# Kernel optimization log

Hardware: AMD Instinct MI355X
Metric: run time of the kernel (lower is better)

## Reference

```python
import math
import jax, jax.numpy as jnp
import numpy as np

D_MODEL = 512
N_HEADS = 8
NUM_PHASES = 3
LN_EPS = 1e-5


def setup_inputs() -> dict:
    key = jax.random.key(0)
    ks = jax.random.split(key, 8)
    B, T, C = 4, 2048, D_MODEL
    s = 1.0 / math.sqrt(C)  # keep activations sane
    return {
        "x": jax.random.normal(ks[0], (B, T, C), dtype=jnp.float32),
        "Wq_w": jax.random.normal(ks[1], (C, C), dtype=jnp.float32) * s,
        "Wq_b": jnp.zeros((C,), dtype=jnp.float32),
        "Wk_w": jax.random.normal(ks[2], (C, C), dtype=jnp.float32) * s,
        "Wk_b": jnp.zeros((C,), dtype=jnp.float32),
        "Wv_w": jax.random.normal(ks[3], (C, C), dtype=jnp.float32) * s,
        "Wv_b": jnp.zeros((C,), dtype=jnp.float32),
        "Wo_w": jax.random.normal(ks[4], (C, C), dtype=jnp.float32) * s,
        "Wo_b": jnp.zeros((C,), dtype=jnp.float32),
        "phase_bias": jax.random.normal(ks[5], (NUM_PHASES, NUM_PHASES), dtype=jnp.float32),
        "ln_g": jnp.ones((C,), dtype=jnp.float32),
        "ln_b": jnp.zeros((C,), dtype=jnp.float32),
    }


def reference(x, Wq_w, Wq_b, Wk_w, Wk_b, Wv_w, Wv_b, Wo_w, Wo_b, phase_bias, ln_g, ln_b):
    B, T, C = x.shape
    H, dk = N_HEADS, C // N_HEADS
    # torch Linear: y = x @ W.T + b
    Q = (x @ Wq_w.T + Wq_b).reshape(B, T, H, dk).transpose(0, 2, 1, 3)
    K = (x @ Wk_w.T + Wk_b).reshape(B, T, H, dk).transpose(0, 2, 1, 3)
    V = (x @ Wv_w.T + Wv_b).reshape(B, T, H, dk).transpose(0, 2, 1, 3)
    scores = jnp.einsum('bhqd,bhkd->bhqk', Q, K) / math.sqrt(dk)  # [B,H,T,T]
    # tiled additive phase bias (num_phases <= T)
    n_tiles = (T + NUM_PHASES - 1) // NUM_PHASES
    bias = jnp.tile(phase_bias, (n_tiles, n_tiles))[:T, :T]  # [T,T]
    scores = scores + bias  # broadcast over B,H
    attn = jax.nn.softmax(scores, axis=-1)  # dropout is identity in eval
    ctx = jnp.einsum('bhqk,bhkd->bhqd', attn, V)
    ctx = ctx.transpose(0, 2, 1, 3).reshape(B, T, C)
    out = ctx @ Wo_w.T + Wo_b
    y = out + x
    mu = jnp.mean(y, axis=-1, keepdims=True)
    var = jnp.mean(jnp.square(y - mu), axis=-1, keepdims=True)
    return (y - mu) / jnp.sqrt(var + LN_EPS) * ln_g + ln_b
```

## Files before the change

### kernel.cpp

```cpp
#include <hip/hip_runtime.h>

typedef __attribute__((ext_vector_type(8))) short s16x8;
typedef __attribute__((ext_vector_type(8))) unsigned short u16x8;
typedef __attribute__((ext_vector_type(4))) float f32x4;
typedef unsigned short u16;
typedef unsigned int u32;

#define T_ 2048
#define C_ 512
#define H_ 8
#define DKP 128
#define LOG2E 1.44269504088896340736f
#define QSCALE 0.18033688011112042f

__device__ __forceinline__ u16 f2b(float f) {
  u32 u = __float_as_uint(f);
  return (u16)((u + 0x7FFFu + ((u >> 16) & 1u)) >> 16);
}

__device__ __forceinline__ float b2f(u16 b) {
  return __uint_as_float(((u32)b) << 16);
}

__device__ __forceinline__ u32 cvtpk(float a, float b) {
  u32 d;
  asm("v_cvt_pk_bf16_f32 %0, %1, %2" : "=v"(d) : "v"(a), "v"(b));
  return d;
}

__device__ __forceinline__ u16x8 cvt8(float4 a, float4 b) {
  u16x8 o;
  o[0] = f2b(a.x); o[1] = f2b(a.y); o[2] = f2b(a.z); o[3] = f2b(a.w);
  o[4] = f2b(b.x); o[5] = f2b(b.y); o[6] = f2b(b.z); o[7] = f2b(b.w);
  return o;
}

__device__ __forceinline__ f32x4 mfma16(s16x8 a, s16x8 b, f32x4 c) {
  return __builtin_amdgcn_mfma_f32_16x16x32_bf16(a, b, c, 0, 0, 0);
}

#define GLL(gp, lp) __builtin_amdgcn_global_load_lds( \
    (const __attribute__((address_space(1))) unsigned int*)(gp), \
    (__attribute__((address_space(3))) unsigned int*)(lp), 16, 0, 0)

__global__ __launch_bounds__(256) void k_convert(
    const float* __restrict__ x,
    const float* __restrict__ wq, const float* __restrict__ wk,
    const float* __restrict__ wv, const float* __restrict__ wo,
    const float* __restrict__ bq, const float* __restrict__ bk,
    const float* __restrict__ bv, const float* __restrict__ pb,
    u16* __restrict__ xb, u16* __restrict__ wcat, u16* __restrict__ wo16,
    float* __restrict__ bcat, u16* __restrict__ qp, u16* __restrict__ kp)
{
  const int blk = blockIdx.x, tid = threadIdx.x;
  if (blk < 2048) {
    int i = blk * 2048 + tid * 8;
    float4 a = *(const float4*)(x + i);
    float4 b = *(const float4*)(x + i + 4);
    *(u16x8*)(xb + i) = cvt8(a, b);
  } else if (blk < 2432) {
    int bi = blk - 2048;
    const float* src; int off;
    if (bi < 128)      { src = wq; off = bi * 2048; }
    else if (bi < 256) { src = wk; off = (bi - 128) * 2048; }
    else               { src = wv; off = (bi - 256) * 2048; }
    int i = off + tid * 8;
    float4 a = *(const float4*)(src + i);
    float4 b = *(const float4*)(src + i + 4);
    *(u16x8*)(wcat + bi * 2048 + tid * 8) = cvt8(a, b);
  } else if (blk < 2560) {
    int i = (blk - 2432) * 2048 + tid * 8;
    float4 a = *(const float4*)(wo + i);
    float4 b = *(const float4*)(wo + i + 4);
    *(u16x8*)(wo16 + i) = cvt8(a, b);
  } else if (blk == 2560) {
    if (tid < 192) {
      int i = tid * 8;
      const float* src; int off;
      if (i < 512)       { src = bq; off = i; }
      else if (i < 1024) { src = bk; off = i - 512; }
      else               { src = bv; off = i - 1024; }
      *(float4*)(bcat + i)     = *(const float4*)(src + off);
      *(float4*)(bcat + i + 4) = *(const float4*)(src + off + 4);
    }
  } else if (blk < 3585) {
    int e = (blk - 2561) * 2048 + tid * 8;
    int row = e >> 5, cc = e & 31;
    int tp = (row & 2047) % 3;
    u16x8 o;
    #pragma unroll
    for (int j = 0; j < 8; ++j) {
      int cidx = cc + j;
      o[j] = (cidx < 3) ? ((tp == cidx) ? (u16)0x3F80 : (u16)0) : (u16)0;
    }
    *(u16x8*)(qp + row * DKP + 64 + cc) = o;
  } else {
    int e = (blk - 3585) * 2048 + tid * 8;
    int row = e >> 5, cc = e & 31;
    int tp = (row & 2047) % 3;
    u16x8 o;
    #pragma unroll
    for (int j = 0; j < 8; ++j) {
      int cidx = cc + j;
      o[j] = (cidx < 3) ? f2b(pb[cidx * 3 + tp] * LOG2E) : (u16)0;
    }
    *(u16x8*)(kp + row * DKP + 64 + cc) = o;
  }
}

template<int MODE>
__global__ __launch_bounds__(256, 2) void k_gemm(
    const u16* __restrict__ A, const u16* __restrict__ Bw,
    const float* __restrict__ bias,
    u16* __restrict__ qp, u16* __restrict__ kp, u16* __restrict__ vtmp,
    float* __restrict__ yout)
{
  const int n0 = blockIdx.x * 128;
  const int m0 = blockIdx.y * 128;
  const int tid = threadIdx.x;
  const int lane = tid & 63, wid = tid >> 6;
  const int g = lane >> 4, c = lane & 15;
  const int wm = wid >> 1, wn = wid & 1;

  __shared__ alignas(16) u16 As[128 * 64];
  __shared__ alignas(16) u16 Bs[128 * 64];

  f32x4 acc[4][4];
  #pragma unroll
  for (int i = 0; i < 4; ++i)
    #pragma unroll
    for (int j = 0; j < 4; ++j) acc[i][j] = f32x4{0.f, 0.f, 0.f, 0.f};

  const int KT = C_ / 64;
  for (int kt = 0; kt < KT; ++kt) {
    #pragma unroll
    for (int i = 0; i < 4; ++i) {
      int ch = i * 256 + tid;
      int row = ch >> 3, col = ch & 7;
      int gcol = (col ^ (row & 7)) << 3;
      GLL(A + (m0 + row) * C_ + kt * 64 + gcol, As + (ch << 3));
      GLL(Bw + (n0 + row) * C_ + kt * 64 + gcol, Bs + (ch << 3));
    }
    __syncthreads();
    #pragma unroll
    for (int ks = 0; ks < 2; ++ks) {
      s16x8 af[4], bf[4];
      #pragma unroll
      for (int mf = 0; mf < 4; ++mf) {
        int row = wm * 64 + mf * 16 + c;
        af[mf] = *(const s16x8*)(As + row * 64 + (((ks * 4 + g) ^ (c & 7)) << 3));
      }
      #pragma unroll
      for (int nf = 0; nf < 4; ++nf) {
        int row = wn * 64 + nf * 16 + c;
        bf[nf] = *(const s16x8*)(Bs + row * 64 + (((ks * 4 + g) ^ (c & 7)) << 3));
      }
      #pragma unroll
      for (int mf = 0; mf < 4; ++mf)
        #pragma unroll
        for (int nf = 0; nf < 4; ++nf)
          acc[mf][nf] = mfma16(af[mf], bf[nf], acc[mf][nf]);
    }
    __syncthreads();
  }

  float bv4[4];
  #pragma unroll
  for (int nf = 0; nf < 4; ++nf) bv4[nf] = bias[n0 + wn * 64 + nf * 16 + c];

  #pragma unroll
  for (int mf = 0; mf < 4; ++mf) {
    const int btb = m0 + wm * 64 + mf * 16 + g * 4;
    #pragma unroll
    for (int nf = 0; nf < 4; ++nf) {
      const int n = n0 + wn * 64 + nf * 16 + c;
      #pragma unroll
      for (int r = 0; r < 4; ++r) {
        float v = acc[mf][nf][r] + bv4[nf];
        const int row = btb + r;
        if (MODE == 1) {
          yout[row * C_ + n] = v;
        } else {
          if (n < 512) {
            const int hh = n >> 6, d = n & 63;
            const int bb = row >> 11, t = row & 2047;
            qp[((bb * H_ + hh) * T_ + t) * DKP + d] = f2b(v * QSCALE);
          } else if (n < 1024) {
            const int nn = n - 512;
            const int hh = nn >> 6, d = nn & 63;
            const int bb = row >> 11, t = row & 2047;
            kp[((bb * H_ + hh) * T_ + t) * DKP + d] = f2b(v);
          } else {
            vtmp[row * C_ + (n - 1024)] = f2b(v);
          }
        }
      }
    }
  }
}

__global__ __launch_bounds__(256) void k_vtrans(const u16* __restrict__ vtmp,
                                                u16* __restrict__ vt)
{
  const int t0 = blockIdx.x * 64;
  const int bh = blockIdx.y;
  const int b = bh >> 3, h = bh & 7;
  const int tid = threadIdx.x;
  __shared__ alignas(16) u16 tile[64 * 72];
  #pragma unroll
  for (int it = 0; it < 2; ++it) {
    int task = tid + it * 256;
    int r = task >> 3, cj = task & 7;
    int pr = (r & 32) | (((r & 15) << 1) | ((r >> 4) & 1));
    u16x8 v = *(const u16x8*)(vtmp + (b * T_ + t0 + r) * C_ + h * 64 + cj * 8);
    #pragma unroll
    for (int j = 0; j < 8; ++j) tile[(cj * 8 + j) * 72 + pr] = v[j];
  }
  __syncthreads();
  #pragma unroll
  for (int it = 0; it < 2; ++it) {
    int task = tid + it * 256;
    int d = task >> 3, cj = task & 7;
    u16x8 o = *(const u16x8*)(tile + d * 72 + cj * 8);
    *(u16x8*)(vt + (bh * 64 + d) * T_ + t0 + cj * 8) = o;
  }
}

__global__ __launch_bounds__(256, 2) void k_attn(
    const u16* __restrict__ qp, const u16* __restrict__ kp,
    const u16* __restrict__ vt, u16* __restrict__ pc0, u16* __restrict__ pc1,
    float* __restrict__ pl)
{
  const int lid = blockIdx.x;
  const int xcd = lid & 7, j = lid >> 3;
  const int gsel = j >> 4, qblk = j & 15;
  const int bhz = xcd * 8 + gsel;
  const int bh = bhz >> 1, z = bhz & 1;

  const int tid = threadIdx.x, wid = tid >> 6, lane = tid & 63;
  const int g = lane >> 4, c = lane & 15;

  __shared__ alignas(16) u16 Kb[2 * 64 * 128];
  __shared__ alignas(16) u16 Vb[2 * 64 * 64];
  __shared__ alignas(16) u16 Pb[4 * 32 * 40];

  const int q0 = qblk * 128 + wid * 32;
  const u16* qpb = qp + ((size_t)bh * T_ + q0) * DKP;
  s16x8 qfr[2][3];
  #pragma unroll
  for (int a = 0; a < 2; ++a)
    #pragma unroll
    for (int ks = 0; ks < 3; ++ks)
      qfr[a][ks] = *(const s16x8*)(qpb + (a * 16 + c) * DKP + ks * 32 + g * 8);

  f32x4 acc[2][5];
  #pragma unroll
  for (int a = 0; a < 2; ++a)
    #pragma unroll
    for (int df = 0; df < 5; ++df) acc[a][df] = f32x4{0.f, 0.f, 0.f, 0.f};

  s16x8 lfrag;
  {
    u16 lv = (c == 0) ? (u16)0x3F80 : (u16)0;
    #pragma unroll
    for (int i = 0; i < 8; ++i) ((u16*)&lfrag)[i] = lv;
  }

  const u16* kpt = kp + ((size_t)bh * T_ + z * 1024) * DKP;
  const u16* vpt = vt + (size_t)bh * 64 * T_ + z * 1024;
  u16* Pw = Pb + wid * (32 * 40);

  auto STAGE = [&](int t, int bsel) {
    const u16* ks0 = kpt + (size_t)t * (64 * DKP);
    u16* kd = Kb + bsel * (64 * 128);
    #pragma unroll
    for (int i = 0; i < 4; ++i) {
      int ch = i * 256 + tid;
      int row = ch >> 4, col = ch & 15;
      GLL(ks0 + row * DKP + ((col ^ (row & 7)) << 3), kd + (ch << 3));
    }
    const u16* vs0 = vpt + t * 64;
    u16* vd = Vb + bsel * (64 * 64);
    #pragma unroll
    for (int i = 0; i < 2; ++i) {
      int ch = i * 256 + tid;
      int row = ch >> 3, col = ch & 7;
      GLL(vs0 + row * T_ + ((col ^ (row & 7)) << 3), vd + (ch << 3));
    }
  };

  STAGE(0, 0);
  __syncthreads();

  for (int kt = 0; kt < 16; ++kt) {
    const int cur = kt & 1;
    if (kt < 15) STAGE(kt + 1, cur ^ 1);

    const u16* Kc = Kb + cur * (64 * 128);
    const u16* Vc = Vb + cur * (64 * 64);

    #pragma unroll
    for (int s = 0; s < 2; ++s) {
      f32x4 s2[2][2];
      #pragma unroll
      for (int a = 0; a < 2; ++a)
        #pragma unroll
        for (int kf = 0; kf < 2; ++kf) s2[a][kf] = f32x4{0.f, 0.f, 0.f, 0.f};
      #pragma unroll
      for (int kf = 0; kf < 2; ++kf)
        #pragma unroll
        for (int ks = 0; ks < 3; ++ks) {
          int row = s * 32 + kf * 16 + c;
          s16x8 kfrag = *(const s16x8*)(Kc + row * 128 +
                                        (((ks * 4 + g) ^ (c & 7)) << 3));
          s2[0][kf] = mfma16(qfr[0][ks], kfrag, s2[0][kf]);
          s2[1][kf] = mfma16(qfr[1][ks], kfrag, s2[1][kf]);
        }

      #pragma unroll
      for (int a = 0; a < 2; ++a) {
        u32* pw = (u32*)Pw + (a * 16 + g * 4) * 20 + c;
        #pragma unroll
        for (int r = 0; r < 4; ++r) {
          float e0 = __builtin_amdgcn_exp2f(s2[a][0][r]);
          float e1 = __builtin_amdgcn_exp2f(s2[a][1][r]);
          pw[r * 20] = cvtpk(e0, e1);
        }
      }

      #pragma unroll
      for (int a = 0; a < 2; ++a) {
        s16x8 pf = *(const s16x8*)(Pw + (a * 16 + c) * 40 + g * 8);
        #pragma unroll
        for (int df = 0; df < 4; ++df) {
          int row = df * 16 + c;
          s16x8 vfrag = *(const s16x8*)(Vc + row * 64 +
                                        (((s * 4 + g) ^ (c & 7)) << 3));
          acc[a][df] = mfma16(pf, vfrag, acc[a][df]);
        }
        acc[a][4] = mfma16(pf, lfrag, acc[a][4]);
      }
    }

    if (kt < 15) __syncthreads();
  }

  u16* pcz = z ? pc1 : pc0;
  float* plz = pl + z * 65536;
  #pragma unroll
  for (int a = 0; a < 2; ++a) {
    #pragma unroll
    for (int r = 0; r < 4; ++r) {
      const int trow = q0 + a * 16 + g * 4 + r;
      u16* outp = pcz + ((size_t)bh * T_ + trow) * 64;
      #pragma unroll
      for (int df = 0; df < 4; ++df)
        outp[df * 16 + c] = f2b(acc[a][df][r]);
      if (c == 0) plz[bh * T_ + trow] = acc[a][4][r];
    }
  }
}

__global__ __launch_bounds__(256) void k_combine(
    const u16* __restrict__ pc0, const u16* __restrict__ pc1,
    const float* __restrict__ pl, u16* __restrict__ ctxb)
{
  const int gid = blockIdx.x * 256 + threadIdx.x;
  const int row = gid >> 3;
  const int dj = (gid & 7) * 8;
  const u16x8 c0 = *(const u16x8*)(pc0 + (size_t)row * 64 + dj);
  const u16x8 c1 = *(const u16x8*)(pc1 + (size_t)row * 64 + dj);
  const float inv = 1.0f / (pl[row] + pl[65536 + row]);
  u16x8 o;
  #pragma unroll
  for (int j = 0; j < 8; ++j)
    o[j] = f2b((b2f(c0[j]) + b2f(c1[j])) * inv);
  const int bh = row >> 11, t = row & 2047;
  const int b = bh >> 3, h = bh & 7;
  *(u16x8*)(ctxb + ((size_t)(b * T_ + t)) * C_ + h * 64 + dj) = o;
}

__global__ __launch_bounds__(256) void k_ln(
    const float* __restrict__ yo, const float* __restrict__ x,
    const float* __restrict__ gg, const float* __restrict__ bb,
    float* __restrict__ out)
{
  const int row = blockIdx.x * 4 + (threadIdx.x >> 6);
  const int lane = threadIdx.x & 63;
  const float4* yp = (const float4*)(yo + row * C_);
  const float4* xp = (const float4*)(x + row * C_);
  float4 v[2];
  float s = 0.f, ss = 0.f;
  #pragma unroll
  for (int i = 0; i < 2; ++i) {
    float4 a = yp[lane * 2 + i];
    float4 xx = xp[lane * 2 + i];
    float4 w;
    w.x = a.x + xx.x; w.y = a.y + xx.y; w.z = a.z + xx.z; w.w = a.w + xx.w;
    v[i] = w;
    s += w.x + w.y + w.z + w.w;
    ss += w.x * w.x + w.y * w.y + w.z * w.z + w.w * w.w;
  }
  #pragma unroll
  for (int m = 1; m < 64; m <<= 1) {
    s += __shfl_xor(s, m);
    ss += __shfl_xor(ss, m);
  }
  const float mu = s * (1.0f / 512.0f);
  const float rs = rsqrtf(ss * (1.0f / 512.0f) - mu * mu + 1e-5f);
  const float4* gp = (const float4*)gg;
  const float4* bp = (const float4*)bb;
  float4* op = (float4*)(out + row * C_);
  #pragma unroll
  for (int i = 0; i < 2; ++i) {
    float4 gv = gp[lane * 2 + i], bv = bp[lane * 2 + i];
    float4 w = v[i], o;
    o.x = (w.x - mu) * rs * gv.x + bv.x;
    o.y = (w.y - mu) * rs * gv.y + bv.y;
    o.z = (w.z - mu) * rs * gv.z + bv.z;
    o.w = (w.w - mu) * rs * gv.w + bv.w;
    op[lane * 2 + i] = o;
  }
}

extern "C" void kernel_launch(void* const* d_in, const int* in_sizes, int n_in,
                              void* d_out, int out_size, void* d_ws, size_t ws_size,
                              hipStream_t stream)
{
  const float* x   = (const float*)d_in[0];
  const float* wqw = (const float*)d_in[1];
  const float* wqb = (const float*)d_in[2];
  const float* wkw = (const float*)d_in[3];
  const float* wkb = (const float*)d_in[4];
  const float* wvw = (const float*)d_in[5];
  const float* wvb = (const float*)d_in[6];
  const float* wow = (const float*)d_in[7];
  const float* wob = (const float*)d_in[8];
  const float* pb  = (const float*)d_in[9];
  const float* lng = (const float*)d_in[10];
  const float* lnb = (const float*)d_in[11];

  char* w = (char*)d_ws;
  u16*   xb   = (u16*)(w + 0);
  u16*   wcat = (u16*)(w + 8388608);
  u16*   wo16 = (u16*)(w + 9961472);
  float* bcat = (float*)(w + 10485760);
  u16*   qp   = (u16*)(w + 10493952);
  u16*   kp   = (u16*)(w + 27271168);
  u16*   vtmp = (u16*)(w + 44048384);
  u16*   vtq  = (u16*)(w + 52436992);
  u16*   pc0  = xb;
  u16*   pc1  = vtmp;
  float* pl   = (float*)wcat;
  u16*   ctxb = kp;
  float* yout = (float*)qp;

  k_convert<<<4609, 256, 0, stream>>>(x, wqw, wkw, wvw, wow, wqb, wkb, wvb, pb,
                                      xb, wcat, wo16, bcat, qp, kp);
  k_gemm<0><<<dim3(12, 64), 256, 0, stream>>>(xb, wcat, bcat, qp, kp, vtmp, nullptr);
  k_vtrans<<<dim3(32, 32), 256, 0, stream>>>(vtmp, vtq);
  k_attn<<<1024, 256, 0, stream>>>(qp, kp, vtq, pc0, pc1, pl);
  k_combine<<<2048, 256, 0, stream>>>(pc0, pc1, pl, ctxb);
  k_gemm<1><<<dim3(4, 64), 256, 0, stream>>>(ctxb, wo16, wob, nullptr, nullptr, nullptr, yout);
  k_ln<<<2048, 256, 0, stream>>>(yout, x, lng, lnb, (float*)d_out);
}
```

Baseline: 201.3 us.

## Fuse split-KV combine into output GEMM, shrink padded head dim, raise attention occupancy

Removes the separate combine kernel by having the output-projection GEMM load both partial context halves and the softmax denominators, normalize them, convert to bf16 and write the A tile straight into shared memory. The padded Q/K row width drops from 128 to 96 elements, cutting Q/K memory traffic and K shared-memory staging, with a new swizzle to match. The attention kernel's launch bounds now ask for 3 blocks per CU. Costs: the GEMM A-load is now synchronous register work instead of async global-to-LDS copies and repeats the normalization for every N tile, and the occupancy hint may force register spills.

```diff
diff --git a/kernel.cpp b/kernel.cpp
--- a/kernel.cpp
+++ b/kernel.cpp
@@ -9,7 +9,7 @@
 #define T_ 2048
 #define C_ 512
 #define H_ 8
-#define DKP 128
+#define DKP 96
 #define LOG2E 1.44269504088896340736f
 #define QSCALE 0.18033688011112042f
 
@@ -26,6 +26,12 @@
   u32 d;
   asm("v_cvt_pk_bf16_f32 %0, %1, %2" : "=v"(d) : "v"(a), "v"(b));
   return d;
+}
+
+__device__ __forceinline__ float rcpf(float x) {
+  float r;
+  asm("v_rcp_f32 %0, %1" : "=v"(r) : "v"(x));
+  return r;
 }
 
 __device__ __forceinline__ u16x8 cvt8(float4 a, float4 b) {
@@ -93,7 +99,7 @@
       int cidx = cc + j;
       o[j] = (cidx < 3) ? ((tp == cidx) ? (u16)0x3F80 : (u16)0) : (u16)0;
     }
-    *(u16x8*)(qp + row * DKP + 64 + cc) = o;
+    *(u16x8*)(qp + (size_t)row * DKP + 64 + cc) = o;
   } else {
     int e = (blk - 3585) * 2048 + tid * 8;
     int row = e >> 5, cc = e & 31;
@@ -104,7 +110,7 @@
       int cidx = cc + j;
       o[j] = (cidx < 3) ? f2b(pb[cidx * 3 + tp] * LOG2E) : (u16)0;
     }
-    *(u16x8*)(kp + row * DKP + 64 + cc) = o;
+    *(u16x8*)(kp + (size_t)row * DKP + 64 + cc) = o;
   }
 }
 
@@ -113,7 +119,9 @@
     const u16* __restrict__ A, const u16* __restrict__ Bw,
     const float* __restrict__ bias,
     u16* __restrict__ qp, u16* __restrict__ kp, u16* __restrict__ vtmp,
-    float* __restrict__ yout)
+    float* __restrict__ yout,
+    const u16* __restrict__ pc0, const u16* __restrict__ pc1,
+    const float* __restrict__ pl)
 {
   const int n0 = blockIdx.x * 128;
   const int m0 = blockIdx.y * 128;
@@ -133,13 +141,41 @@
 
   const int KT = C_ / 64;
   for (int kt = 0; kt < KT; ++kt) {
-    #pragma unroll
-    for (int i = 0; i < 4; ++i) {
-      int ch = i * 256 + tid;
-      int row = ch >> 3, col = ch & 7;
-      int gcol = (col ^ (row & 7)) << 3;
-      GLL(A + (m0 + row) * C_ + kt * 64 + gcol, As + (ch << 3));
-      GLL(Bw + (n0 + row) * C_ + kt * 64 + gcol, Bs + (ch << 3));
+    if (MODE == 0) {
+      #pragma unroll
+      for (int i = 0; i < 4; ++i) {
+        int ch = i * 256 + tid;
+        int row = ch >> 3, col = ch & 7;
+        int gcol = (col ^ (row & 7)) << 3;
+        GLL(A + (m0 + row) * C_ + kt * 64 + gcol, As + (ch << 3));
+        GLL(Bw + (n0 + row) * C_ + kt * 64 + gcol, Bs + (ch << 3));
+      }
+    } else {
+      #pragma unroll
+      for (int i = 0; i < 4; ++i) {
+        int ch = i * 256 + tid;
+        int row = ch >> 3, col = ch & 7;
+        int gcol = (col ^ (row & 7)) << 3;
+        GLL(Bw + (n0 + row) * C_ + kt * 64 + gcol, Bs + (ch << 3));
+      }
+      #pragma unroll
+      for (int i = 0; i < 4; ++i) {
+        int ch = i * 256 + tid;
+        int row = ch >> 3, col = ch & 7;
+        int m = m0 + row;
+        int b = m >> 11, t = m & 2047;
+        int lrow = (b * H_ + kt) * T_ + t;
+        size_t base = (size_t)lrow * 64 + col * 8;
+        u16x8 v0 = *(const u16x8*)(pc0 + base);
+        u16x8 v1 = *(const u16x8*)(pc1 + base);
+        float inv = rcpf(pl[lrow] + pl[65536 + lrow]);
+        u32 wpk[4];
+        #pragma unroll
+        for (int p = 0; p < 4; ++p)
+          wpk[p] = cvtpk((b2f(v0[2 * p]) + b2f(v1[2 * p])) * inv,
+                         (b2f(v0[2 * p + 1]) + b2f(v1[2 * p + 1])) * inv);
+        *(s16x8*)(As + row * 64 + ((col ^ (row & 7)) << 3)) = *(s16x8*)wpk;
+      }
     }
     __syncthreads();
     #pragma unroll
@@ -179,19 +215,19 @@
         float v = acc[mf][nf][r] + bv4[nf];
         const int row = btb + r;
         if (MODE == 1) {
-          yout[row * C_ + n] = v;
+          yout[(size_t)row * C_ + n] = v;
         } else {
           if (n < 512) {
             const int hh = n >> 6, d = n & 63;
             const int bb = row >> 11, t = row & 2047;
-            qp[((bb * H_ + hh) * T_ + t) * DKP + d] = f2b(v * QSCALE);
+            qp[((size_t)(bb * H_ + hh) * T_ + t) * DKP + d] = f2b(v * QSCALE);
           } else if (n < 1024) {
             const int nn = n - 512;
             const int hh = nn >> 6, d = nn & 63;
             const int bb = row >> 11, t = row & 2047;
-            kp[((bb * H_ + hh) * T_ + t) * DKP + d] = f2b(v);
+            kp[((size_t)(bb * H_ + hh) * T_ + t) * DKP + d] = f2b(v);
           } else {
-            vtmp[row * C_ + (n - 1024)] = f2b(v);
+            vtmp[(size_t)row * C_ + (n - 1024)] = f2b(v);
           }
         }
       }
@@ -212,7 +248,7 @@
     int task = tid + it * 256;
     int r = task >> 3, cj = task & 7;
     int pr = (r & 32) | (((r & 15) << 1) | ((r >> 4) & 1));
-    u16x8 v = *(const u16x8*)(vtmp + (b * T_ + t0 + r) * C_ + h * 64 + cj * 8);
+    u16x8 v = *(const u16x8*)(vtmp + (size_t)(b * T_ + t0 + r) * C_ + h * 64 + cj * 8);
     #pragma unroll
     for (int j = 0; j < 8; ++j) tile[(cj * 8 + j) * 72 + pr] = v[j];
   }
@@ -222,25 +258,25 @@
     int task = tid + it * 256;
     int d = task >> 3, cj = task & 7;
     u16x8 o = *(const u16x8*)(tile + d * 72 + cj * 8);
-    *(u16x8*)(vt + (bh * 64 + d) * T_ + t0 + cj * 8) = o;
-  }
-}
-
-__global__ __launch_bounds__(256, 2) void k_attn(
+    *(u16x8*)(vt + (size_t)(bh * 64 + d) * T_ + t0 + cj * 8) = o;
+  }
+}
+
+__global__ __launch_bounds__(256, 3) void k_attn(
     const u16* __restrict__ qp, const u16* __restrict__ kp,
     const u16* __restrict__ vt, u16* __restrict__ pc0, u16* __restrict__ pc1,
     float* __restrict__ pl)
 {
   const int lid = blockIdx.x;
-  const int xcd = lid & 7, j = lid >> 3;
-  const int gsel = j >> 4, qblk = j & 15;
+  const int xcd = lid & 7, jj = lid >> 3;
+  const int gsel = jj >> 4, qblk = jj & 15;
   const int bhz = xcd * 8 + gsel;
   const int bh = bhz >> 1, z = bhz & 1;
 
   const int tid = threadIdx.x, wid = tid >> 6, lane = tid & 63;
   const int g = lane >> 4, c = lane & 15;
 
-  __shared__ alignas(16) u16 Kb[2 * 64 * 128];
+  __shared__ alignas(16) u16 Kb[2 * 64 * 96];
   __shared__ alignas(16) u16 Vb[2 * 64 * 64];
   __shared__ alignas(16) u16 Pb[4 * 32 * 40];
 
@@ -272,12 +308,12 @@
 
   auto STAGE = [&](int t, int bsel) {
     const u16* ks0 = kpt + (size_t)t * (64 * DKP);
-    u16* kd = Kb + bsel * (64 * 128);
-    #pragma unroll
-    for (int i = 0; i < 4; ++i) {
+    u16* kd = Kb + bsel * (64 * 96);
+    #pragma unroll
+    for (int i = 0; i < 3; ++i) {
       int ch = i * 256 + tid;
-      int row = ch >> 4, col = ch & 15;
-      GLL(ks0 + row * DKP + ((col ^ (row & 7)) << 3), kd + (ch << 3));
+      int row = ch / 12, col = ch % 12;
+      GLL(ks0 + row * DKP + ((col ^ ((row >> 1) & 3)) << 3), kd + (ch << 3));
     }
     const u16* vs0 = vpt + t * 64;
     u16* vd = Vb + bsel * (64 * 64);
@@ -296,7 +332,7 @@
     const int cur = kt & 1;
     if (kt < 15) STAGE(kt + 1, cur ^ 1);
 
-    const u16* Kc = Kb + cur * (64 * 128);
+    const u16* Kc = Kb + cur * (64 * 96);
     const u16* Vc = Vb + cur * (64 * 64);
 
     #pragma unroll
@@ -307,15 +343,16 @@
         #pragma unroll
         for (int kf = 0; kf < 2; ++kf) s2[a][kf] = f32x4{0.f, 0.f, 0.f, 0.f};
       #pragma unroll
-      for (int kf = 0; kf < 2; ++kf)
+      for (int kf = 0; kf < 2; ++kf) {
+        const int krow = s * 32 + kf * 16 + c;
         #pragma unroll
         for (int ks = 0; ks < 3; ++ks) {
-          int row = s * 32 + kf * 16 + c;
-          s16x8 kfrag = *(const s16x8*)(Kc + row * 128 +
-                                        (((ks * 4 + g) ^ (c & 7)) << 3));
+          s16x8 kfrag = *(const s16x8*)(Kc + krow * 96 +
+                                        (((ks * 4 + g) ^ ((krow >> 1) & 3)) << 3));
           s2[0][kf] = mfma16(qfr[0][ks], kfrag, s2[0][kf]);
           s2[1][kf] = mfma16(qfr[1][ks], kfrag, s2[1][kf]);
         }
+      }
 
       #pragma unroll
       for (int a = 0; a < 2; ++a) {
@@ -333,9 +370,9 @@
         s16x8 pf = *(const s16x8*)(Pw + (a * 16 + c) * 40 + g * 8);
         #pragma unroll
         for (int df = 0; df < 4; ++df) {
-          int row = df * 16 + c;
-          s16x8 vfrag = *(const s16x8*)(Vc + row * 64 +
-                                        (((s * 4 + g) ^ (c & 7)) << 3));
+          int vrow = df * 16 + c;
+          s16x8 vfrag = *(const s16x8*)(Vc + vrow * 64 +
+                                        (((s * 4 + g) ^ (vrow & 7)) << 3));
           acc[a][df] = mfma16(pf, vfrag, acc[a][df]);
         }
         acc[a][4] = mfma16(pf, lfrag, acc[a][4]);
@@ -359,25 +396,6 @@
       if (c == 0) plz[bh * T_ + trow] = acc[a][4][r];
     }
   }
-}
-
-__global__ __launch_bounds__(256) void k_combine(
-    const u16* __restrict__ pc0, const u16* __restrict__ pc1,
-    const float* __restrict__ pl, u16* __restrict__ ctxb)
-{
-  const int gid = blockIdx.x * 256 + threadIdx.x;
-  const int row = gid >> 3;
-  const int dj = (gid & 7) * 8;
-  const u16x8 c0 = *(const u16x8*)(pc0 + (size_t)row * 64 + dj);
-  const u16x8 c1 = *(const u16x8*)(pc1 + (size_t)row * 64 + dj);
-  const float inv = 1.0f / (pl[row] + pl[65536 + row]);
-  u16x8 o;
-  #pragma unroll
-  for (int j = 0; j < 8; ++j)
-    o[j] = f2b((b2f(c0[j]) + b2f(c1[j])) * inv);
-  const int bh = row >> 11, t = row & 2047;
-  const int b = bh >> 3, h = bh & 7;
-  *(u16x8*)(ctxb + ((size_t)(b * T_ + t)) * C_ + h * 64 + dj) = o;
 }
 
 __global__ __launch_bounds__(256) void k_ln(
@@ -387,8 +405,8 @@
 {
   const int row = blockIdx.x * 4 + (threadIdx.x >> 6);
   const int lane = threadIdx.x & 63;
-  const float4* yp = (const float4*)(yo + row * C_);
-  const float4* xp = (const float4*)(x + row * C_);
+  const float4* yp = (const float4*)(yo + (size_t)row * C_);
+  const float4* xp = (const float4*)(x + (size_t)row * C_);
   float4 v[2];
   float s = 0.f, ss = 0.f;
   #pragma unroll
@@ -410,7 +428,7 @@
   const float rs = rsqrtf(ss * (1.0f / 512.0f) - mu * mu + 1e-5f);
   const float4* gp = (const float4*)gg;
   const float4* bp = (const float4*)bb;
-  float4* op = (float4*)(out + row * C_);
+  float4* op = (float4*)(out + (size_t)row * C_);
   #pragma unroll
   for (int i = 0; i < 2; ++i) {
     float4 gv = gp[lane * 2 + i], bv = bp[lane * 2 + i];
@@ -446,21 +464,21 @@
   u16*   wo16 = (u16*)(w + 9961472);
   float* bcat = (float*)(w + 10485760);
   u16*   qp   = (u16*)(w + 10493952);
-  u16*   kp   = (u16*)(w + 27271168);
-  u16*   vtmp = (u16*)(w + 44048384);
-  u16*   vtq  = (u16*)(w + 52436992);
+  u16*   kp   = (u16*)(w + 23076864);
+  u16*   vtmp = (u16*)(w + 35659776);
+  u16*   vtq  = (u16*)(w + 44048384);
   u16*   pc0  = xb;
   u16*   pc1  = vtmp;
   float* pl   = (float*)wcat;
-  u16*   ctxb = kp;
   float* yout = (float*)qp;
 
   k_convert<<<4609, 256, 0, stream>>>(x, wqw, wkw, wvw, wow, wqb, wkb, wvb, pb,
                                       xb, wcat, wo16, bcat, qp, kp);
-  k_gemm<0><<<dim3(12, 64), 256, 0, stream>>>(xb, wcat, bcat, qp, kp, vtmp, nullptr);
+  k_gemm<0><<<dim3(12, 64), 256, 0, stream>>>(xb, wcat, bcat, qp, kp, vtmp,
+                                              nullptr, nullptr, nullptr, nullptr);
   k_vtrans<<<dim3(32, 32), 256, 0, stream>>>(vtmp, vtq);
   k_attn<<<1024, 256, 0, stream>>>(qp, kp, vtq, pc0, pc1, pl);
-  k_combine<<<2048, 256, 0, stream>>>(pc0, pc1, pl, ctxb);
-  k_gemm<1><<<dim3(4, 64), 256, 0, stream>>>(ctxb, wo16, wob, nullptr, nullptr, nullptr, yout);
+  k_gemm<1><<<dim3(4, 64), 256, 0, stream>>>(nullptr, wo16, wob, nullptr, nullptr,
+                                             nullptr, yout, pc0, pc1, pl);
   k_ln<<<2048, 256, 0, stream>>>(yout, x, lng, lnb, (float*)d_out);
 }
```

After: 217.7 us. +8.1%, slower.
